# Optimization experiments

Measured on AMD Instinct MI355X. Metric: run time of the kernel, lower is better.

The kernel has to match this reference:

```python
import jax, jax.numpy as jnp
import numpy as np

N_VOLS, N_PTS, N_IND = 24, 32768, 18
N_OUT = 144
FEAT_RES = 16
N_FEAT = (N_OUT - N_IND) // 3  # 42
HIDDEN = 32


def setup_inputs() -> dict:
    key = jax.random.key(0)
    ks = jax.random.split(key, 7)
    pts = jax.random.uniform(ks[0], (N_VOLS, N_PTS, 3), jnp.float32, minval=-1.0, maxval=1.0)
    feature = jax.random.normal(ks[1], (N_VOLS, N_FEAT, FEAT_RES, 3), jnp.float32) * 0.1
    ind_feature = jax.random.normal(ks[2], (N_VOLS, N_PTS, N_IND), jnp.float32) * 0.1
    d_in = N_OUT - N_IND  # 126
    w1 = jax.random.normal(ks[3], (N_VOLS, d_in, HIDDEN), jnp.float32) * (1.0 / np.sqrt(d_in))
    b1 = jnp.zeros((N_VOLS, HIDDEN), jnp.float32)
    w2 = jax.random.normal(ks[4], (N_VOLS, HIDDEN, d_in), jnp.float32) * (1.0 / np.sqrt(HIDDEN))
    b2 = jnp.zeros((N_VOLS, d_in), jnp.float32)
    return {"pts": pts, "feature": feature, "ind_feature": ind_feature,
            "w1": w1, "b1": b1, "w2": w2, "b2": b2}


def _factorize_grid_sample(feature, pts):
    # feature: (J, F, R, 3) per-axis line features; pts: (J, P, 3) in [-1, 1]
    # returns (J, P, 3, F): 1D linear interp of axis-c line at pts[..., c] (align_corners=True)
    J, Fc, R, C = feature.shape
    x = jnp.clip((pts + 1.0) * 0.5 * (R - 1), 0.0, R - 1)  # (J,P,3)
    x0 = jnp.clip(jnp.floor(x).astype(jnp.int32), 0, R - 2)
    w = x - x0.astype(x.dtype)
    # flatten (J,R,C,F) so a single gather fetches all F channels per (j,p,c)
    feat_flat = feature.transpose(0, 2, 3, 1).reshape(J * R * C, Fc)
    base = (jnp.arange(J)[:, None, None] * R + x0) * C + jnp.arange(C)[None, None, :]  # (J,P,3)
    g0 = feat_flat[base]        # (J,P,3,F)
    g1 = feat_flat[base + C]    # next grid point along R
    return g0 + w[..., None] * (g1 - g0)


def reference(pts, feature, ind_feature, w1, b1, w2, b2):
    J, Fc, R, C = feature.shape
    P = pts.shape[1]
    g = _factorize_grid_sample(feature, pts)              # (J,P,3,F)
    # rearrange 'j f p c -> p j (f c)' : (J,P,C,F) -> (P,J,F,C) -> (P,J,F*C)
    v = g.transpose(1, 0, 3, 2).reshape(P, J, Fc * C)
    # per-volume 2-layer MLP (ParallelLinear -> ReLU -> ParallelLinear)
    h = jax.nn.relu(jnp.einsum('pji,jio->pjo', v, w1) + b1)
    o = jnp.einsum('pji,jio->pjo', h, w2) + b2            # (P,J,F*C)
    o = o.transpose(1, 0, 2)                              # (J,P,F*C)
    return jnp.concatenate([ind_feature, o], axis=-1)     # (J,P,n_out)
```

## Files before the change

### kernel.cpp

```cpp
#include <hip/hip_runtime.h>

#define NVOLS 24
#define NPTS  32768
#define NIND  18
#define NFEAT 42
#define RES   16
#define HID   32
#define DIN   126
#define NOUTC 144

#define TPB   256
#define PPB   256
#define BLOCKS_PER_VOL (NPTS / PPB)
#define CHUNK 64
#define NCHUNK (PPB / CHUNK)

#define SFEAT_N     (3 * NFEAT * RES)
#define SHHC_STRIDE 33
#define SHHC_N      (CHUNK * SHHC_STRIDE)
#define SOUT_STRIDE 127
#define SOUT_N      (CHUNK * SOUT_STRIDE)
#define SIND_N      (CHUNK * NIND)

typedef float f4 __attribute__((ext_vector_type(4)));

__global__ __launch_bounds__(TPB, 3) void fused_gridsample_mlp(
    const float* __restrict__ pts,
    const float* __restrict__ feature,
    const float* __restrict__ ind,
    const float* __restrict__ w1,
    const float* __restrict__ b1,
    const float* __restrict__ w2,
    const float* __restrict__ b2,
    float* __restrict__ out)
{
    __shared__ float sfeat[SFEAT_N];
    __shared__ float sh_hc[SHHC_N];
    __shared__ float sh_out[SOUT_N];
    __shared__ float sh_ind[SIND_N];

    const int tid   = threadIdx.x;
    const int j     = blockIdx.x / BLOCKS_PER_VOL;
    const int pbase = (blockIdx.x % BLOCKS_PER_VOL) * PPB;

    const float* fj = feature + j * (NFEAT * RES * 3);
    for (int e = tid; e < SFEAT_N; e += TPB) {
        int f   = e / (RES * 3);
        int rem = e - f * (RES * 3);
        int r   = rem / 3;
        int c   = rem - r * 3;
        sfeat[(c * NFEAT + f) * RES + r] = fj[e];
    }

    const int p = pbase + tid;
    float wfr[3]; int xb[3];
    {
        const float* pp = pts + (size_t)(j * NPTS + p) * 3;
        #pragma unroll
        for (int c = 0; c < 3; c++) {
            float x = (pp[c] + 1.0f) * 7.5f;
            x = fminf(fmaxf(x, 0.0f), 15.0f);
            int x0 = (int)x;
            x0 = min(x0, RES - 2);
            wfr[c] = x - (float)x0;
            xb[c]  = c * (NFEAT * RES) + x0;
        }
    }
    __syncthreads();

    const float* w1j = w1 + j * (DIN * HID);
    const float* b1j = b1 + j * HID;
    float h[HID];
    #pragma unroll
    for (int o = 0; o < HID; o++) h[o] = b1j[o];

    for (int f = 0; f < NFEAT; f++) {
        #pragma unroll
        for (int c = 0; c < 3; c++) {
            int   idx = xb[c] + f * RES;
            float g0  = sfeat[idx];
            float g1  = sfeat[idx + 1];
            float v   = fmaf(wfr[c], g1 - g0, g0);
            const float* wrow = w1j + (f * 3 + c) * HID;
            #pragma unroll
            for (int o = 0; o < HID; o++)
                h[o] = fmaf(v, wrow[o], h[o]);
        }
    }
    #pragma unroll
    for (int o = 0; o < HID; o++) h[o] = fmaxf(h[o], 0.0f);

    const float* w2j = w2 + j * (HID * DIN);
    const float* b2j = b2 + j * DIN;
    const int wave = tid >> 6;
    const int psub = tid & 63;
    const int k0 = __builtin_amdgcn_readfirstlane((tid >> 6) * 32);

    for (int c = 0; c < NCHUNK; c++) {
        if (wave == c) {
            #pragma unroll
            for (int o = 0; o < HID; o++)
                sh_hc[psub * SHHC_STRIDE + o] = h[o];
        }
        __syncthreads();

        const float* indc = ind + (size_t)(j * NPTS + pbase + c * CHUNK) * NIND;
        #pragma unroll
        for (int i2 = 0; i2 < 3; i2++) {
            int f2 = i2 * TPB + tid;
            if (f2 < CHUNK * NIND / 2) {
                float2 v = ((const float2*)indc)[f2];
                sh_ind[f2 * 2]     = v.x;
                sh_ind[f2 * 2 + 1] = v.y;
            }
        }

        float acc[32];
        #pragma unroll
        for (int kk = 0; kk < 32; kk++) {
            int kc = min(k0 + kk, DIN - 1);
            acc[kk] = b2j[kc];
        }
        #pragma unroll 4
        for (int o = 0; o < HID; o++) {
            float hho = sh_hc[psub * SHHC_STRIDE + o];
            const float* wrow = w2j + o * DIN;
            #pragma unroll
            for (int kk = 0; kk < 32; kk++) {
                int kc = min(k0 + kk, DIN - 1);
                acc[kk] = fmaf(hho, wrow[kc], acc[kk]);
            }
        }
        #pragma unroll
        for (int kk = 0; kk < 32; kk++) {
            int k = k0 + kk;
            if (k < DIN)
                sh_out[psub * SOUT_STRIDE + k] = acc[kk];
        }
        __syncthreads();

        float* outc = out + (size_t)(j * NPTS + pbase + c * CHUNK) * NOUTC;
        #pragma unroll
        for (int i = 0; i < (CHUNK * NOUTC / 4) / TPB; i++) {
            int flat4 = i * TPB + tid;
            int pr = flat4 / 36;
            int q  = flat4 - pr * 36;
            f4 v;
            if (q < 4) {
                int b = pr * NIND + 4 * q;
                v = (f4){sh_ind[b], sh_ind[b + 1], sh_ind[b + 2], sh_ind[b + 3]};
            } else if (q == 4) {
                int b = pr * NIND + 16;
                int s = pr * SOUT_STRIDE;
                v = (f4){sh_ind[b], sh_ind[b + 1], sh_out[s], sh_out[s + 1]};
            } else {
                int s = pr * SOUT_STRIDE + (4 * q - NIND);
                v = (f4){sh_out[s], sh_out[s + 1], sh_out[s + 2], sh_out[s + 3]};
            }
            __builtin_nontemporal_store(v, (f4*)outc + flat4);
        }
        __syncthreads();
    }
}

extern "C" void kernel_launch(void* const* d_in, const int* in_sizes, int n_in,
                              void* d_out, int out_size, void* d_ws, size_t ws_size,
                              hipStream_t stream) {
    const float* pts     = (const float*)d_in[0];
    const float* feature = (const float*)d_in[1];
    const float* ind     = (const float*)d_in[2];
    const float* w1      = (const float*)d_in[3];
    const float* b1      = (const float*)d_in[4];
    const float* w2      = (const float*)d_in[5];
    const float* b2      = (const float*)d_in[6];
    float* out           = (float*)d_out;

    dim3 grid(NVOLS * BLOCKS_PER_VOL);
    dim3 block(TPB);
    fused_gridsample_mlp<<<grid, block, 0, stream>>>(pts, feature, ind, w1, b1, w2, b2, out);
}
```

Measured before the change: 799.4 us.

## Specialize layer-2 slices per wave and write ind_feature directly to output

Layer 2 is now split into templated per-wave slices with compile-time offsets, which removes the clamped-index bias and weight loads and the guarded stores for the last wave. The ind_feature tile is copied straight from global memory to the output with float2 stores instead of being staged in shared memory. The MLP results are written with float2 stores in place of the nontemporal float4 stores, and one barrier per chunk is removed. In exchange the output uses narrower, ordinary cached stores, and dropping the trailing barrier could introduce a race between the next chunk's writes to sh_hc/sh_out and the reads of the current chunk.

```diff
diff --git a/kernel.cpp b/kernel.cpp
--- a/kernel.cpp
+++ b/kernel.cpp
@@ -20,9 +20,25 @@
 #define SHHC_N      (CHUNK * SHHC_STRIDE)
 #define SOUT_STRIDE 127
 #define SOUT_N      (CHUNK * SOUT_STRIDE)
-#define SIND_N      (CHUNK * NIND)
 
-typedef float f4 __attribute__((ext_vector_type(4)));
+template<int K0, int KLEN>
+__device__ __forceinline__ void layer2_slice(
+    const float* __restrict__ w2j, const float* __restrict__ b2j,
+    const float* hrow, float* orow)
+{
+    float acc[KLEN];
+    #pragma unroll
+    for (int kk = 0; kk < KLEN; kk++) acc[kk] = b2j[K0 + kk];
+    #pragma unroll
+    for (int o = 0; o < HID; o++) {
+        float hho = hrow[o];
+        #pragma unroll
+        for (int kk = 0; kk < KLEN; kk++)
+            acc[kk] = fmaf(hho, w2j[o * DIN + K0 + kk], acc[kk]);
+    }
+    #pragma unroll
+    for (int kk = 0; kk < KLEN; kk++) orow[K0 + kk] = acc[kk];
+}
 
 __global__ __launch_bounds__(TPB, 3) void fused_gridsample_mlp(
     const float* __restrict__ pts,
@@ -37,7 +53,6 @@
     __shared__ float sfeat[SFEAT_N];
     __shared__ float sh_hc[SHHC_N];
     __shared__ float sh_out[SOUT_N];
-    __shared__ float sh_ind[SIND_N];
 
     const int tid   = threadIdx.x;
     const int j     = blockIdx.x / BLOCKS_PER_VOL;
@@ -94,7 +109,7 @@
     const float* b2j = b2 + j * DIN;
     const int wave = tid >> 6;
     const int psub = tid & 63;
-    const int k0 = __builtin_amdgcn_readfirstlane((tid >> 6) * 32);
+    const int wv = __builtin_amdgcn_readfirstlane(wave);
 
     for (int c = 0; c < NCHUNK; c++) {
         if (wave == c) {
@@ -104,62 +119,45 @@
         }
         __syncthreads();
 
-        const float* indc = ind + (size_t)(j * NPTS + pbase + c * CHUNK) * NIND;
-        #pragma unroll
-        for (int i2 = 0; i2 < 3; i2++) {
-            int f2 = i2 * TPB + tid;
-            if (f2 < CHUNK * NIND / 2) {
-                float2 v = ((const float2*)indc)[f2];
-                sh_ind[f2 * 2]     = v.x;
-                sh_ind[f2 * 2 + 1] = v.y;
-            }
+        {
+            const float* hrow = sh_hc + psub * SHHC_STRIDE;
+            float* orow = sh_out + psub * SOUT_STRIDE;
+            if      (wv == 0) layer2_slice< 0, 32>(w2j, b2j, hrow, orow);
+            else if (wv == 1) layer2_slice<32, 32>(w2j, b2j, hrow, orow);
+            else if (wv == 2) layer2_slice<64, 32>(w2j, b2j, hrow, orow);
+            else              layer2_slice<96, 30>(w2j, b2j, hrow, orow);
         }
 
-        float acc[32];
-        #pragma unroll
-        for (int kk = 0; kk < 32; kk++) {
-            int kc = min(k0 + kk, DIN - 1);
-            acc[kk] = b2j[kc];
-        }
-        #pragma unroll 4
-        for (int o = 0; o < HID; o++) {
-            float hho = sh_hc[psub * SHHC_STRIDE + o];
-            const float* wrow = w2j + o * DIN;
+        {
+            const float* indc = ind + (size_t)(j * NPTS + pbase + c * CHUNK) * NIND;
+            float* outc = out + (size_t)(j * NPTS + pbase + c * CHUNK) * NOUTC;
             #pragma unroll
-            for (int kk = 0; kk < 32; kk++) {
-                int kc = min(k0 + kk, DIN - 1);
-                acc[kk] = fmaf(hho, wrow[kc], acc[kk]);
+            for (int i = 0; i < 3; i++) {
+                int u = i * TPB + tid;
+                if (u < CHUNK * NIND / 2) {
+                    float2 v = ((const float2*)indc)[u];
+                    int pr = u / 9;
+                    int m  = u - pr * 9;
+                    *(float2*)(outc + pr * NOUTC + 2 * m) = v;
+                }
             }
-        }
-        #pragma unroll
-        for (int kk = 0; kk < 32; kk++) {
-            int k = k0 + kk;
-            if (k < DIN)
-                sh_out[psub * SOUT_STRIDE + k] = acc[kk];
         }
         __syncthreads();
 
-        float* outc = out + (size_t)(j * NPTS + pbase + c * CHUNK) * NOUTC;
-        #pragma unroll
-        for (int i = 0; i < (CHUNK * NOUTC / 4) / TPB; i++) {
-            int flat4 = i * TPB + tid;
-            int pr = flat4 / 36;
-            int q  = flat4 - pr * 36;
-            f4 v;
-            if (q < 4) {
-                int b = pr * NIND + 4 * q;
-                v = (f4){sh_ind[b], sh_ind[b + 1], sh_ind[b + 2], sh_ind[b + 3]};
-            } else if (q == 4) {
-                int b = pr * NIND + 16;
-                int s = pr * SOUT_STRIDE;
-                v = (f4){sh_ind[b], sh_ind[b + 1], sh_out[s], sh_out[s + 1]};
-            } else {
-                int s = pr * SOUT_STRIDE + (4 * q - NIND);
-                v = (f4){sh_out[s], sh_out[s + 1], sh_out[s + 2], sh_out[s + 3]};
+        {
+            float* outc = out + (size_t)(j * NPTS + pbase + c * CHUNK) * NOUTC;
+            #pragma unroll 4
+            for (int i = 0; i < 16; i++) {
+                int u = i * TPB + tid;
+                if (u < CHUNK * (DIN / 2)) {
+                    int pr = u / 63;
+                    int m  = u - pr * 63;
+                    float a0 = sh_out[pr * SOUT_STRIDE + 2 * m];
+                    float a1 = sh_out[pr * SOUT_STRIDE + 2 * m + 1];
+                    *(float2*)(outc + pr * NOUTC + NIND + 2 * m) = make_float2(a0, a1);
+                }
             }
-            __builtin_nontemporal_store(v, (f4*)outc + flat4);
         }
-        __syncthreads();
     }
 }
 
```

After: 785.4 us. No clear change (-1.7%).
